# Kernel optimization log

Measured on AMD Instinct MI355X. Metric: run time of the kernel, lower is better.

## Reference

```python
import jax, jax.numpy as jnp
import numpy as np

IN_FEATURES = 512
NUM_TREES = 512
DEPTH = 6
RESPONSE_DIM = 3
NLEAF = 2 ** DEPTH  # 64
BATCH = 1024


def _make_path_map():
    # OBLIVIOUS_map from DeTree.InitPathWay: nodes = range(depth);
    # for leaf `no`, path[j] = 2*nodes[j] + ((no >> j) & 1)
    pm = np.array([[2 * j + ((no >> j) & 1) for j in range(DEPTH)]
                   for no in range(NLEAF)], dtype=np.int32)
    return jnp.asarray(pm.reshape(-1))  # [NLEAF*DEPTH]


def setup_inputs() -> dict:
    key = jax.random.key(0)
    k1, k2, k3, k4, k5 = jax.random.split(key, 5)
    x = jax.random.normal(k1, (BATCH, IN_FEATURES), dtype=jnp.float32)
    # feat_attention initialized with nn.init.uniform_ in the original
    feat_attention = jax.random.uniform(k2, (IN_FEATURES, NUM_TREES * DEPTH), dtype=jnp.float32)
    thresholds = jax.random.normal(k3, (NUM_TREES, DEPTH), dtype=jnp.float32)
    log_temperatures = jax.random.normal(k4, (NUM_TREES, DEPTH), dtype=jnp.float32) * 0.1
    response = jax.random.normal(k5, (NUM_TREES, NLEAF, RESPONSE_DIM), dtype=jnp.float32)
    return {
        "x": x,
        "feat_attention": feat_attention,
        "thresholds": thresholds,
        "log_temperatures": log_temperatures,
        "response": response,
        "path_map": _make_path_map(),
    }


def reference(x, feat_attention, thresholds, log_temperatures, response, path_map):
    B = x.shape[0]
    # choice_function over features (dim=0), then view [F, T, D]
    choice_weight = jax.nn.softmax(feat_attention, axis=0)
    choice_weight = choice_weight.reshape(IN_FEATURES, NUM_TREES, DEPTH)
    # feature_values: [B, T, D]
    feature_values = jnp.einsum('bf,fnd->bnd', x, choice_weight)
    # threshold + temperature, sparsemoid bin function: clip(0.5*t + 0.5, 0, 1)
    t = (feature_values - thresholds[None]) * jnp.exp(-log_temperatures)[None]
    bins = jnp.clip(0.5 * t + 0.5, 0.0, 1.0)  # [B, T, D]
    # gate outputs indexed by 2*node + left_right: interleave bins / 1-bins
    gates = jnp.stack([bins, 1.0 - bins], axis=-1).reshape(B, NUM_TREES, 2 * DEPTH)
    # irregular gather routing via path_map: [B, T, NLEAF*DEPTH] -> [B, T, NLEAF, D]
    pathed = jnp.take(gates, path_map, axis=2).reshape(B, NUM_TREES, NLEAF, DEPTH)
    response_weights = jnp.prod(pathed, axis=-1)  # [B, T, NLEAF]
    out = jnp.einsum('bnl,nlr->bnr', response_weights, response)  # [B, T, R]
    return out.reshape(B, NUM_TREES * RESPONSE_DIM)
```

## Files before the change

### kernel.cpp

```cpp
#include <hip/hip_runtime.h>

#define F 512
#define T 512
#define DEPTH 6
#define NL 64
#define NCOL 3072

typedef __attribute__((ext_vector_type(8))) short short8v;
typedef __attribute__((ext_vector_type(4))) float float4v;

static __device__ __forceinline__ unsigned short f2bf(float f){
  unsigned u = __builtin_bit_cast(unsigned, f);
  unsigned r = (u + 0x7fffu + ((u >> 16) & 1u)) >> 16;
  return (unsigned short)r;
}

static __device__ __forceinline__ void glds16(const unsigned short* g, char* lds){
  __builtin_amdgcn_global_load_lds(
      (const __attribute__((address_space(1))) unsigned int*)(uintptr_t)(const void*)g,
      (__attribute__((address_space(3))) unsigned int*)(uintptr_t)(void*)lds,
      16, 0, 0);
}

__global__ __launch_bounds__(256) void k_prep(const float* __restrict__ fa,
                                              const float* __restrict__ x,
                                              unsigned short* __restrict__ xb,
                                              unsigned short* __restrict__ cwT,
                                              float* __restrict__ partial){
  __shared__ float tile[64 * 65];
  __shared__ float red[4][64];
  int t = threadIdx.x, c = t & 63, q = t >> 6;
  int n0 = blockIdx.x * 64, k0 = blockIdx.y * 64;

  int gid = (blockIdx.y * 48 + blockIdx.x) * 256 + t;
  for (int i = gid; i < 131072; i += 98304){
    float4 v = ((const float4*)x)[i];
    ushort4 o;
    o.x = f2bf(v.x); o.y = f2bf(v.y); o.z = f2bf(v.z); o.w = f2bf(v.w);
    ((ushort4*)xb)[i] = o;
  }

  float s = 0.f;
  #pragma unroll
  for (int i = 0; i < 16; ++i){
    int kk = q * 16 + i;
    float e = __expf(fa[(k0 + kk) * NCOL + n0 + c]);
    tile[c * 65 + kk] = e;
    s += e;
  }
  red[q][c] = s;
  __syncthreads();
  if (t < 64)
    partial[blockIdx.y * NCOL + n0 + t] = red[0][t] + red[1][t] + red[2][t] + red[3][t];

  #pragma unroll
  for (int j = 0; j < 2; ++j){
    int s2 = t + 256 * j;
    int nn = s2 >> 3, ko = s2 & 7;
    const float* tp = tile + nn * 65 + ko * 8;
    unsigned short tmp[8];
    #pragma unroll
    for (int z = 0; z < 8; ++z) tmp[z] = f2bf(tp[z]);
    *(int4*)(cwT + (n0 + nn) * F + k0 + ko * 8) = *(const int4*)tmp;
  }
}

#define AB0 0
#define AB1 8192
#define BB0 16384
#define BB1 28672
#define RSP_OFF 40960
#define RSP_STRIDE 260
#define SL_OFF (40960 + 16640)
#define SMEM3 (40960 + 16640 + 384)
__global__ __launch_bounds__(256) void k_main(
    const unsigned short* __restrict__ xb, const unsigned short* __restrict__ cwT,
    const float* __restrict__ thr, const float* __restrict__ ltm,
    const float* __restrict__ resp, const float* __restrict__ partial,
    float* __restrict__ out){
  __shared__ char smem[SMEM3];
  float* fvl = (float*)smem;
  float* rsp = (float*)(smem + RSP_OFF);
  float* sL  = (float*)(smem + SL_OFF);

  int t = threadIdx.x;
  int wg = blockIdx.x;
  int sid = (wg & 7) * 64 + (wg >> 3);
  int bx = sid & 15, ty = sid >> 4;
  int b0 = bx * 64;
  int t0 = ty * 16, n0 = ty * 96;

  int w = t >> 6, l = t & 63;
  int wm = w >> 1, wn = w & 1;
  int lr = l & 15, lg = l >> 4;
  int lrow8 = l >> 3;
  int lswz = ((l & 7) ^ lrow8) << 3;

  const unsigned short* gA0 = xb  + (b0 + w * 16 + 0 + lrow8) * F + lswz;
  const unsigned short* gA1 = xb  + (b0 + w * 16 + 8 + lrow8) * F + lswz;
  const unsigned short* gB0 = cwT + (n0 + w * 24 + 0 + lrow8) * F + lswz;
  const unsigned short* gB1 = cwT + (n0 + w * 24 + 8 + lrow8) * F + lswz;
  const unsigned short* gB2 = cwT + (n0 + w * 24 + 16 + lrow8) * F + lswz;
  int lA = w * 16 * 128;
  int lB = w * 24 * 128;

  glds16(gA0, smem + AB0 + lA);
  glds16(gA1, smem + AB0 + lA + 1024);
  glds16(gB0, smem + BB0 + lB);
  glds16(gB1, smem + BB0 + lB + 1024);
  glds16(gB2, smem + BB0 + lB + 2048);

  if (t < 96){
    float s = 0.f;
    #pragma unroll
    for (int i = 0; i < 8; ++i) s += partial[i * NCOL + n0 + t];
    sL[t] = 1.0f / s;
  }
  {
    const float4* rg = (const float4*)(resp + t0 * (NL * 3));
    #pragma unroll
    for (int j = 0; j < 3; ++j){
      int s = t + 256 * j;
      int tr = s / 48, m0 = (s % 48) * 4;
      float4 v = rg[s];
      float vv[4] = {v.x, v.y, v.z, v.w};
      #pragma unroll
      for (int z = 0; z < 4; ++z){
        int m = m0 + z;
        rsp[tr * RSP_STRIDE + (m / 3) * 4 + (m % 3)] = vv[z];
      }
    }
  }

  float4v acc[2][3];
  #pragma unroll
  for (int i = 0; i < 2; ++i)
    #pragma unroll
    for (int j = 0; j < 3; ++j) acc[i][j] = (float4v){0.f,0.f,0.f,0.f};

  __syncthreads();

  int swz = (lr & 7) << 4;
  #pragma unroll
  for (int cc = 0; cc < 8; ++cc){
    char* Ab = smem + ((cc & 1) ? AB1 : AB0);
    char* Bb = smem + ((cc & 1) ? BB1 : BB0);
    if (cc < 7){
      int kc = (cc + 1) * 64;
      char* An = smem + ((cc & 1) ? AB0 : AB1);
      char* Bn = smem + ((cc & 1) ? BB0 : BB1);
      glds16(gA0 + kc, An + lA);
      glds16(gA1 + kc, An + lA + 1024);
      glds16(gB0 + kc, Bn + lB);
      glds16(gB1 + kc, Bn + lB + 1024);
      glds16(gB2 + kc, Bn + lB + 2048);
    }
    if (cc < 7) asm volatile("s_waitcnt vmcnt(5)" ::: "memory");
    else        asm volatile("s_waitcnt vmcnt(0)" ::: "memory");
    asm volatile("s_barrier" ::: "memory");
    char* Ar = Ab + (wm * 32 + lr) * 128;
    char* Br = Bb + (wn * 48 + lr) * 128;
    #pragma unroll
    for (int ks = 0; ks < 2; ++ks){
      int ko = (ks * 64 + lg * 16) ^ swz;
      short8v a0 = *(const short8v*)(Ar + ko);
      short8v a1 = *(const short8v*)(Ar + 2048 + ko);
      short8v b0 = *(const short8v*)(Br + ko);
      short8v b1 = *(const short8v*)(Br + 2048 + ko);
      short8v b2 = *(const short8v*)(Br + 4096 + ko);
      acc[0][0] = __builtin_amdgcn_mfma_f32_16x16x32_bf16(a0, b0, acc[0][0], 0, 0, 0);
      acc[0][1] = __builtin_amdgcn_mfma_f32_16x16x32_bf16(a0, b1, acc[0][1], 0, 0, 0);
      acc[0][2] = __builtin_amdgcn_mfma_f32_16x16x32_bf16(a0, b2, acc[0][2], 0, 0, 0);
      acc[1][0] = __builtin_amdgcn_mfma_f32_16x16x32_bf16(a1, b0, acc[1][0], 0, 0, 0);
      acc[1][1] = __builtin_amdgcn_mfma_f32_16x16x32_bf16(a1, b1, acc[1][1], 0, 0, 0);
      acc[1][2] = __builtin_amdgcn_mfma_f32_16x16x32_bf16(a1, b2, acc[1][2], 0, 0, 0);
    }
    asm volatile("s_barrier" ::: "memory");
  }

  float sf0 = sL[wn * 48 + lr];
  float sf1 = sL[wn * 48 + 16 + lr];
  float sf2 = sL[wn * 48 + 32 + lr];
  #pragma unroll
  for (int fm = 0; fm < 2; ++fm)
    #pragma unroll
    for (int r = 0; r < 4; ++r){
      int m = wm * 32 + fm * 16 + lg * 4 + r;
      fvl[m * 100 + wn * 48 + lr]      = acc[fm][0][r] * sf0;
      fvl[m * 100 + wn * 48 + 16 + lr] = acc[fm][1][r] * sf1;
      fvl[m * 100 + wn * 48 + 32 + lr] = acc[fm][2][r] * sf2;
    }
  __syncthreads();

  int tl = t & 15, bl0 = t >> 4;
  const float* thp = thr + (t0 + tl) * 6;
  const float* ltp = ltm + (t0 + tl) * 6;
  float av[DEPTH], cv[DEPTH];
  #pragma unroll
  for (int d = 0; d < DEPTH; ++d){
    av[d] = 0.5f * __expf(-ltp[d]);
    cv[d] = 0.5f - thp[d] * av[d];
  }
  float wv[4][16], qq[4][4];
  #pragma unroll
  for (int p = 0; p < 4; ++p){
    int bl = bl0 + 16 * p;
    float bn[DEPTH];
    #pragma unroll
    for (int d = 0; d < DEPTH; ++d)
      bn[d] = fminf(fmaxf(fvl[bl * 100 + tl * 6 + d] * av[d] + cv[d], 0.0f), 1.0f);
    wv[p][0] = bn[0]; wv[p][1] = 1.0f - bn[0];
    #pragma unroll
    for (int j = 1; j < 4; ++j){
      int half = 1 << j;
      float g = bn[j];
      #pragma unroll
      for (int i = 0; i < half; ++i){
        float o = wv[p][i];
        wv[p][i] = o * g;
        wv[p][i + half] = o - wv[p][i];
      }
    }
    float p4 = bn[4], p5 = bn[5];
    qq[p][0] = p4 * p5;
    qq[p][1] = (1.0f - p4) * p5;
    qq[p][2] = p4 * (1.0f - p5);
    qq[p][3] = (1.0f - p4) * (1.0f - p5);
  }
  float4v oa[4];
  #pragma unroll
  for (int p = 0; p < 4; ++p) oa[p] = (float4v){0.f,0.f,0.f,0.f};
  const float* rp = rsp + tl * RSP_STRIDE;
  #pragma unroll
  for (int i = 0; i < 16; ++i){
    float4v r0  = *(const float4v*)(rp + i * 4);
    float4v r16 = *(const float4v*)(rp + (i + 16) * 4);
    float4v r32 = *(const float4v*)(rp + (i + 32) * 4);
    float4v r48 = *(const float4v*)(rp + (i + 48) * 4);
    #pragma unroll
    for (int p = 0; p < 4; ++p){
      float4v s = r0 * qq[p][0] + r16 * qq[p][1] + r32 * qq[p][2] + r48 * qq[p][3];
      oa[p] += s * wv[p][i];
    }
  }
  #pragma unroll
  for (int p = 0; p < 4; ++p){
    float* op = out + (b0 + bl0 + 16 * p) * (T * 3) + (t0 + tl) * 3;
    op[0] = oa[p][0]; op[1] = oa[p][1]; op[2] = oa[p][2];
  }
}

extern "C" void kernel_launch(void* const* d_in, const int* in_sizes, int n_in,
                              void* d_out, int out_size, void* d_ws, size_t ws_size,
                              hipStream_t stream){
  const float* x    = (const float*)d_in[0];
  const float* fa   = (const float*)d_in[1];
  const float* thr  = (const float*)d_in[2];
  const float* ltm  = (const float*)d_in[3];
  const float* resp = (const float*)d_in[4];
  float* out = (float*)d_out;

  unsigned short* cwT = (unsigned short*)d_ws;
  unsigned short* xb  = (unsigned short*)((char*)d_ws + (3 << 20));
  float* partial      = (float*)((char*)d_ws + (4 << 20));

  k_prep<<<dim3(48, 8), 256, 0, stream>>>(fa, x, xb, cwT, partial);
  k_main<<<512, 256, 0, stream>>>(xb, cwT, thr, ltm, resp, partial, out);
}
```

Measured before the change: 21.48 us.

## Double batch tile per workgroup to 128 rows with 512-thread blocks

Each k_main workgroup now covers 128 batch rows instead of 64, using 8 waves (512 threads), so the grid shrinks from 512 to 256 blocks. The B tile (chosen-weight columns) is now loaded once per 128 rows, halving redundant B traffic and LDS fills per output row. Load assignment, vmcnt waits, LDS offsets and the epilogue row strides are rebalanced, with some waves issuing one fewer B load. In exchange the grid is smaller, per-block LDS use is larger, and only one block fits per CU, which may reduce latency hiding.

After: 21.08 us. Within noise of the previous version (-1.9%).

```diff
diff --git a/kernel.cpp b/kernel.cpp
--- a/kernel.cpp
+++ b/kernel.cpp
@@ -66,28 +66,28 @@
 }
 
 #define AB0 0
-#define AB1 8192
-#define BB0 16384
-#define BB1 28672
-#define RSP_OFF 40960
+#define AB1 16384
+#define BB0 32768
+#define BB1 45056
+#define SL_OFF 57344
+#define RSP_OFF 57728
 #define RSP_STRIDE 260
-#define SL_OFF (40960 + 16640)
-#define SMEM3 (40960 + 16640 + 384)
-__global__ __launch_bounds__(256) void k_main(
+#define SMEM3 (57728 + 16640)
+__global__ __launch_bounds__(512) void k_main(
     const unsigned short* __restrict__ xb, const unsigned short* __restrict__ cwT,
     const float* __restrict__ thr, const float* __restrict__ ltm,
     const float* __restrict__ resp, const float* __restrict__ partial,
     float* __restrict__ out){
   __shared__ char smem[SMEM3];
   float* fvl = (float*)smem;
+  float* sL  = (float*)(smem + SL_OFF);
   float* rsp = (float*)(smem + RSP_OFF);
-  float* sL  = (float*)(smem + SL_OFF);
 
   int t = threadIdx.x;
   int wg = blockIdx.x;
-  int sid = (wg & 7) * 64 + (wg >> 3);
-  int bx = sid & 15, ty = sid >> 4;
-  int b0 = bx * 64;
+  int sid = (wg & 7) * 32 + (wg >> 3);
+  int bx = sid & 7, ty = sid >> 3;
+  int b0 = bx * 128;
   int t0 = ty * 16, n0 = ty * 96;
 
   int w = t >> 6, l = t & 63;
@@ -96,19 +96,16 @@
   int lrow8 = l >> 3;
   int lswz = ((l & 7) ^ lrow8) << 3;
 
-  const unsigned short* gA0 = xb  + (b0 + w * 16 + 0 + lrow8) * F + lswz;
-  const unsigned short* gA1 = xb  + (b0 + w * 16 + 8 + lrow8) * F + lswz;
-  const unsigned short* gB0 = cwT + (n0 + w * 24 + 0 + lrow8) * F + lswz;
-  const unsigned short* gB1 = cwT + (n0 + w * 24 + 8 + lrow8) * F + lswz;
-  const unsigned short* gB2 = cwT + (n0 + w * 24 + 16 + lrow8) * F + lswz;
+  const unsigned short* gA = xb + (b0 + w * 16 + lrow8) * F + lswz;
+  int bB = (w < 4) ? (w * 16) : (64 + 8 * (w - 4));
+  const unsigned short* gB = cwT + (n0 + bB + lrow8) * F + lswz;
   int lA = w * 16 * 128;
-  int lB = w * 24 * 128;
-
-  glds16(gA0, smem + AB0 + lA);
-  glds16(gA1, smem + AB0 + lA + 1024);
-  glds16(gB0, smem + BB0 + lB);
-  glds16(gB1, smem + BB0 + lB + 1024);
-  glds16(gB2, smem + BB0 + lB + 2048);
+  int lB = bB * 128;
+
+  glds16(gA, smem + AB0 + lA);
+  glds16(gA + 8 * F, smem + AB0 + lA + 1024);
+  glds16(gB, smem + BB0 + lB);
+  if (w < 4) glds16(gB + 8 * F, smem + BB0 + lB + 1024);
 
   if (t < 96){
     float s = 0.f;
@@ -119,15 +116,17 @@
   {
     const float4* rg = (const float4*)(resp + t0 * (NL * 3));
     #pragma unroll
-    for (int j = 0; j < 3; ++j){
-      int s = t + 256 * j;
-      int tr = s / 48, m0 = (s % 48) * 4;
-      float4 v = rg[s];
-      float vv[4] = {v.x, v.y, v.z, v.w};
-      #pragma unroll
-      for (int z = 0; z < 4; ++z){
-        int m = m0 + z;
-        rsp[tr * RSP_STRIDE + (m / 3) * 4 + (m % 3)] = vv[z];
+    for (int j = 0; j < 2; ++j){
+      int s = t + 512 * j;
+      if (s < 768){
+        int tr = s / 48, m0 = (s % 48) * 4;
+        float4 v = rg[s];
+        float vv[4] = {v.x, v.y, v.z, v.w};
+        #pragma unroll
+        for (int z = 0; z < 4; ++z){
+          int m = m0 + z;
+          rsp[tr * RSP_STRIDE + (m / 3) * 4 + (m % 3)] = vv[z];
+        }
       }
     }
   }
@@ -149,14 +148,17 @@
       int kc = (cc + 1) * 64;
       char* An = smem + ((cc & 1) ? AB0 : AB1);
       char* Bn = smem + ((cc & 1) ? BB0 : BB1);
-      glds16(gA0 + kc, An + lA);
-      glds16(gA1 + kc, An + lA + 1024);
-      glds16(gB0 + kc, Bn + lB);
-      glds16(gB1 + kc, Bn + lB + 1024);
-      glds16(gB2 + kc, Bn + lB + 2048);
-    }
-    if (cc < 7) asm volatile("s_waitcnt vmcnt(5)" ::: "memory");
-    else        asm volatile("s_waitcnt vmcnt(0)" ::: "memory");
+      glds16(gA + kc, An + lA);
+      glds16(gA + kc + 8 * F, An + lA + 1024);
+      glds16(gB + kc, Bn + lB);
+      if (w < 4) glds16(gB + kc + 8 * F, Bn + lB + 1024);
+    }
+    if (cc < 7){
+      if (w < 4) asm volatile("s_waitcnt vmcnt(4)" ::: "memory");
+      else       asm volatile("s_waitcnt vmcnt(3)" ::: "memory");
+    } else {
+      asm volatile("s_waitcnt vmcnt(0)" ::: "memory");
+    }
     asm volatile("s_barrier" ::: "memory");
     char* Ar = Ab + (wm * 32 + lr) * 128;
     char* Br = Bb + (wn * 48 + lr) * 128;
@@ -204,7 +206,7 @@
   float wv[4][16], qq[4][4];
   #pragma unroll
   for (int p = 0; p < 4; ++p){
-    int bl = bl0 + 16 * p;
+    int bl = bl0 + 32 * p;
     float bn[DEPTH];
     #pragma unroll
     for (int d = 0; d < DEPTH; ++d)
@@ -245,7 +247,7 @@
   }
   #pragma unroll
   for (int p = 0; p < 4; ++p){
-    float* op = out + (b0 + bl0 + 16 * p) * (T * 3) + (t0 + tl) * 3;
+    float* op = out + (b0 + bl0 + 32 * p) * (T * 3) + (t0 + tl) * 3;
     op[0] = oa[p][0]; op[1] = oa[p][1]; op[2] = oa[p][2];
   }
 }
@@ -265,5 +267,5 @@
   float* partial      = (float*)((char*)d_ws + (4 << 20));
 
   k_prep<<<dim3(48, 8), 256, 0, stream>>>(fa, x, xb, cwT, partial);
-  k_main<<<512, 256, 0, stream>>>(xb, cwT, thr, ltm, resp, partial, out);
-}
+  k_main<<<256, 512, 0, stream>>>(xb, cwT, thr, ltm, resp, partial, out);
+}
```
